# Optimization experiments

Measured on AMD Instinct MI355X. Metric: run time of the kernel, lower is better.

## Reference

```python
import jax, jax.numpy as jnp
import numpy as np


def l2norm(t, eps=1e-12):
    # matches F.normalize(p=2, dim=-1): divide by norm clamped to eps
    n = jnp.linalg.norm(t, axis=-1, keepdims=True)
    return t / jnp.maximum(n, eps)


def setup_inputs() -> dict:
    key = jax.random.key(0)
    kx, ke = jax.random.split(key)
    B, N, D, C = 8, 1024, 256, 8192
    x = jax.random.normal(kx, (B, N, D), dtype=jnp.float32)
    # codebook initialized l2-normalized, as in __init__ (kmeans_init=False)
    embed = l2norm(jax.random.normal(ke, (1, C, D), dtype=jnp.float32))
    return {"x": x, "embed": embed}


def reference(x, embed):
    # x: [B, N, D]; ndim < 4 -> add codebook dim h=1
    xh = x[None]                                   # [1, B, N, D]
    h, b, n, d = xh.shape
    flat = l2norm(xh.reshape(h, b * n, d))         # [1, B*N, D]
    e = l2norm(embed)                              # [1, C, D]
    # cosine-similarity distances
    dist = jnp.einsum('hnd,hcd->hnc', flat, e)     # [1, B*N, C]
    # sample_codebook_temp == 0 -> plain argmax
    idx = jnp.argmax(dist, axis=-1).reshape(h, b, n)  # [1, B, N]
    # batched_embedding: gather UN-normalized codebook rows
    quantize = jax.vmap(lambda em, ix: em[ix])(embed, idx)  # [1, B, N, D]
    # needs_codebook_dim -> strip leading dim
    return quantize[0], idx[0]
```

## Files before the change

### kernel.cpp

```cpp
#include <hip/hip_runtime.h>
#include <math.h>

#define QROWS 8192
#define DDIM  256
#define CCNT  8192

typedef __attribute__((ext_vector_type(4))) float f32x4;
typedef __attribute__((ext_vector_type(8))) short bf16x8;

__device__ __forceinline__ unsigned short f2bf(float f) {
    unsigned u = __float_as_uint(f);
    u += 0x7fffu + ((u >> 16) & 1u);
    return (unsigned short)(u >> 16);
}
__device__ __forceinline__ unsigned u32max(unsigned a, unsigned b) { return a > b ? a : b; }
__device__ __forceinline__ unsigned u32min(unsigned a, unsigned b) { return a < b ? a : b; }

__device__ __forceinline__ unsigned key32(float v, unsigned enc) {
    unsigned u = __float_as_uint(v);
    unsigned s = (unsigned)((int)u >> 31);
    return ((u ^ (s | 0x80000000u)) & 0xFFFFFF00u) | enc;
}

__global__ void k_prep(const float* __restrict__ x, unsigned short* __restrict__ xb,
                       const float* __restrict__ e, unsigned short* __restrict__ eb) {
    const int bid = blockIdx.x;
    if (bid < 1024) {
        const int i = (bid * 256 + threadIdx.x) * 8;
        const float4 f0 = *reinterpret_cast<const float4*>(x + i);
        const float4 f1 = *reinterpret_cast<const float4*>(x + i + 4);
        uint4 o;
        o.x = f2bf(f0.x) | ((unsigned)f2bf(f0.y) << 16);
        o.y = f2bf(f0.z) | ((unsigned)f2bf(f0.w) << 16);
        o.z = f2bf(f1.x) | ((unsigned)f2bf(f1.y) << 16);
        o.w = f2bf(f1.z) | ((unsigned)f2bf(f1.w) << 16);
        *reinterpret_cast<uint4*>(xb + i) = o;
    } else {
        const int row  = (bid - 1024) * 4 + (threadIdx.x >> 6);
        const int lane = threadIdx.x & 63;
        const float4 v = *reinterpret_cast<const float4*>(e + (size_t)row * DDIM + lane * 4);
        float s = v.x * v.x + v.y * v.y + v.z * v.z + v.w * v.w;
        #pragma unroll
        for (int off = 1; off < 64; off <<= 1) s += __shfl_xor(s, off);
        const float inv = 1.0f / fmaxf(sqrtf(s), 1e-12f);
        ushort4 o;
        o.x = f2bf(v.x * inv); o.y = f2bf(v.y * inv);
        o.z = f2bf(v.z * inv); o.w = f2bf(v.w * inv);
        *reinterpret_cast<ushort4*>(eb + (size_t)row * DDIM + lane * 4) = o;
    }
}

#define GLOAD_LDS(g, s) \
    __builtin_amdgcn_global_load_lds((const __attribute__((address_space(1))) void*)(g), \
                                     (__attribute__((address_space(3))) void*)(s), 16, 0, 0)

#define SBAR do { asm volatile("" ::: "memory"); __builtin_amdgcn_s_barrier(); \
                  asm volatile("" ::: "memory"); } while (0)
#define WAIT_LGKM(n) do { asm volatile("s_waitcnt lgkmcnt(" #n ")" ::: "memory"); \
                          __builtin_amdgcn_sched_barrier(0); } while (0)
#define WAIT_VM(n) do { asm volatile("s_waitcnt vmcnt(" #n ")" ::: "memory"); \
                        __builtin_amdgcn_sched_barrier(0); } while (0)

__launch_bounds__(512, 2)
__global__ void k_gemm(const unsigned short* __restrict__ xb,
                       const unsigned short* __restrict__ eb,
                       unsigned* pout ) {
    extern __shared__ char smem[];

    const int tid = threadIdx.x;
    const int w = tid >> 6, l = tid & 63;
    const int lg = l >> 4, lr = l & 15;
    const int bid = blockIdx.x;
    const int panel = (bid & 7) * 2 + ((bid >> 3) >> 4);
    const int split = (bid >> 3) & 15;
    const int n0 = panel * 512, c0 = split * 512;

    const int arl = w * 2 + (l >> 5);
    const size_t soff = (size_t)(((l & 31) ^ (arl & 7)) * 16);
    const char* gApro = (const char*)xb + (size_t)(n0 + arl) * 512 + soff;
    const char* gBpro = (const char*)eb + (size_t)(c0 + arl) * 512 + soff;
    const int wlds = w * 1024;

#define STAGEA(r) do { _Pragma("unroll") for (int g_ = 0; g_ < 4; ++g_)                    \
    GLOAD_LDS(gApro + (r) * 32768 + g_ * 8192,                                             \
              smem + ((r) & 1) * 32768 + g_ * 8192 + wlds); } while (0)
#define STAGEB(t) do { _Pragma("unroll") for (int g_ = 0; g_ < 2; ++g_)                    \
    GLOAD_LDS(gBpro + (size_t)(t) * 16384 + g_ * 8192,                                     \
              smem + 65536 + ((t) & 3) * 16384 + g_ * 8192 + wlds); } while (0)

    bf16x8 aF[4][8];
#define READA(slot) do { _Pragma("unroll") for (int mi_ = 0; mi_ < 4; ++mi_)               \
    _Pragma("unroll") for (int kk_ = 0; kk_ < 8; ++kk_)                                    \
        aF[mi_][kk_] = *reinterpret_cast<const bf16x8*>(smem + (slot) * 32768              \
            + (mi_ * 16 + lr) * 512 + (((kk_ * 4 + lg) ^ (lr & 7)) * 16)); } while (0)

    STAGEA(0); STAGEA(1);
    STAGEB(0); STAGEB(1); STAGEB(2); STAGEB(3);
    WAIT_VM(12); SBAR;  if (w == 0) READA(0);  WAIT_LGKM(0); SBAR; STAGEA(2);
    WAIT_VM(12); SBAR;  if (w == 1) READA(1);  WAIT_LGKM(0); SBAR; STAGEA(3);
    WAIT_VM(4);  SBAR;  if (w == 2) READA(0);  WAIT_LGKM(0); SBAR; STAGEA(4);
    WAIT_VM(4);  SBAR;  if (w == 3) READA(1);  WAIT_LGKM(0); SBAR; STAGEA(5);
    WAIT_VM(4);  SBAR;  if (w == 4) READA(0);  WAIT_LGKM(0); SBAR; STAGEA(6);
    WAIT_VM(4);  SBAR;  if (w == 5) READA(1);  WAIT_LGKM(0); SBAR; STAGEA(7);
    WAIT_VM(4);  SBAR;  if (w == 6) READA(0);  WAIT_LGKM(0); SBAR;
    WAIT_VM(0);  SBAR;  if (w == 7) READA(1);  WAIT_LGKM(0); SBAR;

    const f32x4 zf4 = {0.f, 0.f, 0.f, 0.f};
    f32x4 acc[4][2];
    #pragma unroll
    for (int i = 0; i < 4; ++i) { acc[i][0] = zf4; acc[i][1] = zf4; }
    unsigned rk1[16], rk2[16];
    #pragma unroll
    for (int i = 0; i < 16; ++i) { rk1[i] = 0u; rk2[i] = 0u; }
    bf16x8 bf[3][2];
    const int bcol0 = lr * 512;
    const int cxor = lr & 7;

#define FLUSH(half) do {                                                                   \
    _Pragma("unroll") for (int i_ = 0; i_ < 16; ++i_) {                                    \
        unsigned t1_ = rk1[i_], t2_ = rk2[i_];                                             \
        _Pragma("unroll") for (int off_ = 1; off_ < 16; off_ <<= 1) {                      \
            const unsigned o1_ = __shfl_xor(t1_, off_);                                    \
            const unsigned o2_ = __shfl_xor(t2_, off_);                                    \
            const unsigned n1_ = u32max(t1_, o1_), lo_ = u32min(t1_, o1_);                 \
            t2_ = u32max(u32max(t2_, o2_), lo_);                                           \
            t1_ = n1_;                                                                     \
        }                                                                                  \
        if (lr == 0) {                                                                     \
            const int row_ = n0 + w * 64 + (i_ >> 2) * 16 + lg * 4 + (i_ & 3);             \
            uint2 o_; o_.x = t1_; o_.y = t2_;                                              \
            *reinterpret_cast<uint2*>(pout + (size_t)row_ * 256 + split * 4 + (half) * 2) = o_; \
        }                                                                                  \
        rk1[i_] = 0u; rk2[i_] = 0u;                                                        \
    }                                                                                      \
} while (0)

    #pragma unroll 1
    for (int t = 0; t < 16; ++t) {
        if (t <= 13)      { WAIT_VM(4); }
        else if (t == 14) { WAIT_VM(2); }
        else              { WAIT_VM(0); }
        SBAR;
        if (t >= 1 && t < 13) STAGEB(t + 3);

        const char* sb = smem + 65536 + (t & 3) * 16384;
        #pragma unroll
        for (int nj = 0; nj < 2; ++nj)
            bf[0][nj] = *reinterpret_cast<const bf16x8*>(sb + nj * 8192 + bcol0 + ((lg ^ cxor) * 16));
        #pragma unroll
        for (int nj = 0; nj < 2; ++nj)
            bf[1][nj] = *reinterpret_cast<const bf16x8*>(sb + nj * 8192 + bcol0 + (((4 + lg) ^ cxor) * 16));

        #pragma unroll
        for (int kk = 0; kk < 8; ++kk) {
            if (kk < 6) {
                #pragma unroll
                for (int nj = 0; nj < 2; ++nj)
                    bf[(kk + 2) % 3][nj] = *reinterpret_cast<const bf16x8*>(
                        sb + nj * 8192 + bcol0 + ((((kk + 2) * 4 + lg) ^ cxor) * 16));
                WAIT_LGKM(4);
            } else if (kk == 6) { WAIT_LGKM(2); } else { WAIT_LGKM(0); }
            __builtin_amdgcn_s_setprio(1);
            #pragma unroll
            for (int mi = 0; mi < 4; ++mi)
                #pragma unroll
                for (int nj = 0; nj < 2; ++nj)
                    acc[mi][nj] = __builtin_amdgcn_mfma_f32_16x16x32_bf16(
                        aF[mi][kk], bf[kk % 3][nj], acc[mi][nj], 0, 0, 0);
            __builtin_amdgcn_s_setprio(0);
        }

        const unsigned encb = (unsigned)(255 - (t & 7) * 32) - (unsigned)lr;
        #pragma unroll
        for (int mi = 0; mi < 4; ++mi)
            #pragma unroll
            for (int rr = 0; rr < 4; ++rr) {
                const unsigned q0 = key32(acc[mi][0][rr], encb);
                const unsigned q1 = key32(acc[mi][1][rr], encb - 16u);
                const unsigned m01 = u32max(q0, q1), n01 = u32min(q0, q1);
                const int i = mi * 4 + rr;
                const unsigned lo = u32min(rk1[i], m01);
                rk1[i] = u32max(rk1[i], m01);
                rk2[i] = u32max(u32max(rk2[i], n01), lo);
                acc[mi][0][rr] = 0.0f; acc[mi][1][rr] = 0.0f;
            }
        if (t == 7) FLUSH(0);
        if (t == 15) FLUSH(1);
    }
#undef STAGEA
#undef STAGEB
#undef READA
#undef FLUSH
}

__global__ void k_fixup(const unsigned* pk,
                        const float* __restrict__ x, const float* __restrict__ e,
                        float* out) {
    const int row = blockIdx.x * 4 + (threadIdx.x >> 6);
    const int t   = threadIdx.x & 63;
    unsigned long long kk0 = 0ull, kk1 = 0ull;
    if (t < 32) {
        const uint2 kv = reinterpret_cast<const uint2*>(pk + (size_t)row * 256)[t];
        const int col0 = t * 256 + 255 - (int)(kv.x & 255u);
        kk0 = ((unsigned long long)(kv.x & 0xFFFFFF00u) << 32) | (unsigned)(~col0);
        const int col1 = t * 256 + 255 - (int)(kv.y & 255u);
        kk1 = ((unsigned long long)(kv.y & 0xFFFFFF00u) << 32) | (unsigned)(~col1);
    }

    int cand[4];
    #pragma unroll
    for (int p = 0; p < 4; ++p) {
        unsigned long long m = kk0 > kk1 ? kk0 : kk1;
        #pragma unroll
        for (int off = 1; off < 64; off <<= 1) {
            const unsigned long long o = __shfl_xor(m, off);
            if (o > m) m = o;
        }
        cand[p] = (int)(~(unsigned)m) & (CCNT - 1);
        if (kk0 == m) kk0 = 0ull;
        if (kk1 == m) kk1 = 0ull;
    }

    const float4 xv = *reinterpret_cast<const float4*>(x + (size_t)row * DDIM + t * 4);
    float best = -INFINITY; int bc = 0x7fffffff;
    #pragma unroll
    for (int p = 0; p < 4; ++p) {
        const int c = cand[p];
        const float4 ev = *reinterpret_cast<const float4*>(e + (size_t)c * DDIM + t * 4);
        float d  = xv.x * ev.x + xv.y * ev.y + xv.z * ev.z + xv.w * ev.w;
        float ss = ev.x * ev.x + ev.y * ev.y + ev.z * ev.z + ev.w * ev.w;
        #pragma unroll
        for (int off = 1; off < 64; off <<= 1) {
            d  += __shfl_xor(d, off);
            ss += __shfl_xor(ss, off);
        }
        const float v = d * (1.0f / fmaxf(sqrtf(ss), 1e-12f));
        if (v > best || (v == best && c < bc)) { best = v; bc = c; }
    }

    if (t == 0) out[(size_t)QROWS * DDIM + row] = (float)bc;
    const float4 q = *reinterpret_cast<const float4*>(e + (size_t)bc * DDIM + t * 4);
    *reinterpret_cast<float4*>(out + (size_t)row * DDIM + t * 4) = q;
}

extern "C" void kernel_launch(void* const* d_in, const int* in_sizes, int n_in,
                              void* d_out, int out_size, void* d_ws, size_t ws_size,
                              hipStream_t stream) {
    const float* x = (const float*)d_in[0];
    const float* e = (const float*)d_in[1];
    float* out = (float*)d_out;
    char* ws = (char*)d_ws;

    unsigned short* xb = (unsigned short*)ws;
    unsigned short* eb = (unsigned short*)(ws + (size_t)4 * 1024 * 1024);

    hipFuncSetAttribute(reinterpret_cast<const void*>(k_gemm),
                        hipFuncAttributeMaxDynamicSharedMemorySize, 131072);

    k_prep<<<3072, 256, 0, stream>>>(x, xb, e, eb);
    k_gemm<<<256, 512, 131072, stream>>>(xb, eb, (unsigned*)d_out);
    k_fixup<<<QROWS / 4, 256, 0, stream>>>((const unsigned*)d_out, x, e, out);
}
```

Baseline: 65.26 us.

## Restructure GEMM staging: two-phase A preload, 8-slot B ring, two tiles per barrier

Replaces the eight-step staggered A-fragment preload with two bulk half-loads that reuse the whole LDS, then turns all 128KB of LDS into an 8-slot ring for codebook (B) tiles. The main loop now handles two B tiles per barrier, with six tiles prefetched ahead, and drops the explicit register triple-buffering, lgkm waits and setprio around the MFMAs. The goal is fewer barriers and deeper global-load prefetch, at the cost of a serialized A-load prologue and leaving LDS-read scheduling to the compiler.

```diff
diff --git a/kernel.cpp b/kernel.cpp
--- a/kernel.cpp
+++ b/kernel.cpp
@@ -69,52 +69,72 @@
 
     const int tid = threadIdx.x;
     const int w = tid >> 6, l = tid & 63;
-    const int lg = l >> 4, lr = l & 15;
+    const int lg = l >> 4, lr = l & 15, lr7 = lr & 7;
     const int bid = blockIdx.x;
     const int panel = (bid & 7) * 2 + ((bid >> 3) >> 4);
     const int split = (bid >> 3) & 15;
     const int n0 = panel * 512, c0 = split * 512;
 
-    const int arl = w * 2 + (l >> 5);
-    const size_t soff = (size_t)(((l & 31) ^ (arl & 7)) * 16);
-    const char* gApro = (const char*)xb + (size_t)(n0 + arl) * 512 + soff;
-    const char* gBpro = (const char*)eb + (size_t)(c0 + arl) * 512 + soff;
-    const int wlds = w * 1024;
-
-#define STAGEA(r) do { _Pragma("unroll") for (int g_ = 0; g_ < 4; ++g_)                    \
-    GLOAD_LDS(gApro + (r) * 32768 + g_ * 8192,                                             \
-              smem + ((r) & 1) * 32768 + g_ * 8192 + wlds); } while (0)
+    const int lchk = (tid & 24) | ((tid & 7) ^ ((tid >> 5) & 7));
+    const char* baseA = (const char*)xb + (size_t)(n0 + (tid >> 5)) * 512 + lchk * 16;
+    const char* baseB = (const char*)eb + (size_t)(c0 + (tid >> 5)) * 512 + lchk * 16;
+    const int wl16 = w * 1024;
+
+#define STAGE_AHALF(h) do { _Pragma("unroll") for (int g_ = 0; g_ < 16; ++g_)              \
+    GLOAD_LDS(baseA + (h) * 131072 + g_ * 8192, smem + g_ * 8192 + wl16); } while (0)
 #define STAGEB(t) do { _Pragma("unroll") for (int g_ = 0; g_ < 2; ++g_)                    \
-    GLOAD_LDS(gBpro + (size_t)(t) * 16384 + g_ * 8192,                                     \
-              smem + 65536 + ((t) & 3) * 16384 + g_ * 8192 + wlds); } while (0)
+    GLOAD_LDS(baseB + (size_t)(t) * 16384 + g_ * 8192,                                     \
+              smem + ((t) & 7) * 16384 + g_ * 8192 + wl16); } while (0)
 
     bf16x8 aF[4][8];
-#define READA(slot) do { _Pragma("unroll") for (int mi_ = 0; mi_ < 4; ++mi_)               \
-    _Pragma("unroll") for (int kk_ = 0; kk_ < 8; ++kk_)                                    \
-        aF[mi_][kk_] = *reinterpret_cast<const bf16x8*>(smem + (slot) * 32768              \
-            + (mi_ * 16 + lr) * 512 + (((kk_ * 4 + lg) ^ (lr & 7)) * 16)); } while (0)
-
-    STAGEA(0); STAGEA(1);
-    STAGEB(0); STAGEB(1); STAGEB(2); STAGEB(3);
-    WAIT_VM(12); SBAR;  if (w == 0) READA(0);  WAIT_LGKM(0); SBAR; STAGEA(2);
-    WAIT_VM(12); SBAR;  if (w == 1) READA(1);  WAIT_LGKM(0); SBAR; STAGEA(3);
-    WAIT_VM(4);  SBAR;  if (w == 2) READA(0);  WAIT_LGKM(0); SBAR; STAGEA(4);
-    WAIT_VM(4);  SBAR;  if (w == 3) READA(1);  WAIT_LGKM(0); SBAR; STAGEA(5);
-    WAIT_VM(4);  SBAR;  if (w == 4) READA(0);  WAIT_LGKM(0); SBAR; STAGEA(6);
-    WAIT_VM(4);  SBAR;  if (w == 5) READA(1);  WAIT_LGKM(0); SBAR; STAGEA(7);
-    WAIT_VM(4);  SBAR;  if (w == 6) READA(0);  WAIT_LGKM(0); SBAR;
-    WAIT_VM(0);  SBAR;  if (w == 7) READA(1);  WAIT_LGKM(0); SBAR;
+#define READA() do { _Pragma("unroll") for (int mi_ = 0; mi_ < 4; ++mi_)                   \
+    _Pragma("unroll") for (int kk_ = 0; kk_ < 8; ++kk_) {                                  \
+        const int lc_ = kk_ * 4 + lg;                                                      \
+        const int ph_ = (lc_ & 24) | ((lc_ & 7) ^ lr7);                                    \
+        aF[mi_][kk_] = *reinterpret_cast<const bf16x8*>(                                   \
+            smem + ((w & 3) * 64 + mi_ * 16 + lr) * 512 + ph_ * 16); } } while (0)
+
+    STAGE_AHALF(0);
+    WAIT_VM(0); SBAR;
+    if (w < 4) READA();
+    WAIT_LGKM(0); SBAR;
+    STAGE_AHALF(1);
+    WAIT_VM(0); SBAR;
+    if (w >= 4) READA();
+    WAIT_LGKM(0); SBAR;
+    STAGEB(0); STAGEB(1); STAGEB(2); STAGEB(3); STAGEB(4); STAGEB(5);
 
     const f32x4 zf4 = {0.f, 0.f, 0.f, 0.f};
     f32x4 acc[4][2];
-    #pragma unroll
-    for (int i = 0; i < 4; ++i) { acc[i][0] = zf4; acc[i][1] = zf4; }
     unsigned rk1[16], rk2[16];
     #pragma unroll
     for (int i = 0; i < 16; ++i) { rk1[i] = 0u; rk2[i] = 0u; }
-    bf16x8 bf[3][2];
-    const int bcol0 = lr * 512;
-    const int cxor = lr & 7;
+
+#define TILE(t) do {                                                                       \
+    const char* sb_ = smem + ((t) & 7) * 16384;                                            \
+    _Pragma("unroll") for (int mi_ = 0; mi_ < 4; ++mi_)                                    \
+        { acc[mi_][0] = zf4; acc[mi_][1] = zf4; }                                          \
+    _Pragma("unroll") for (int kk_ = 0; kk_ < 8; ++kk_) {                                  \
+        const int lc_ = kk_ * 4 + lg;                                                      \
+        const int ph_ = ((lc_ & 24) | ((lc_ & 7) ^ lr7)) * 16;                             \
+        const bf16x8 b0_ = *reinterpret_cast<const bf16x8*>(sb_ + (lr) * 512 + ph_);       \
+        const bf16x8 b1_ = *reinterpret_cast<const bf16x8*>(sb_ + (16 + lr) * 512 + ph_);  \
+        _Pragma("unroll") for (int mi_ = 0; mi_ < 4; ++mi_) {                              \
+            acc[mi_][0] = __builtin_amdgcn_mfma_f32_16x16x32_bf16(aF[mi_][kk_], b0_, acc[mi_][0], 0, 0, 0); \
+            acc[mi_][1] = __builtin_amdgcn_mfma_f32_16x16x32_bf16(aF[mi_][kk_], b1_, acc[mi_][1], 0, 0, 0); \
+        } }                                                                                \
+    const unsigned encb_ = (unsigned)(255 - ((t) & 7) * 32) - (unsigned)lr;                \
+    _Pragma("unroll") for (int mi_ = 0; mi_ < 4; ++mi_)                                    \
+        _Pragma("unroll") for (int rr_ = 0; rr_ < 4; ++rr_) {                              \
+            const unsigned q0_ = key32(acc[mi_][0][rr_], encb_);                           \
+            const unsigned q1_ = key32(acc[mi_][1][rr_], encb_ - 16u);                     \
+            const unsigned m01_ = u32max(q0_, q1_), n01_ = u32min(q0_, q1_);               \
+            const int i_ = mi_ * 4 + rr_;                                                  \
+            const unsigned lo_ = u32min(rk1[i_], m01_);                                    \
+            rk1[i_] = u32max(rk1[i_], m01_);                                               \
+            rk2[i_] = u32max(u32max(rk2[i_], n01_), lo_);                                  \
+        }                                                                                  \
+} while (0)
 
 #define FLUSH(half) do {                                                                   \
     _Pragma("unroll") for (int i_ = 0; i_ < 16; ++i_) {                                    \
@@ -136,60 +156,21 @@
 } while (0)
 
     #pragma unroll 1
-    for (int t = 0; t < 16; ++t) {
-        if (t <= 13)      { WAIT_VM(4); }
-        else if (t == 14) { WAIT_VM(2); }
-        else              { WAIT_VM(0); }
+    for (int u = 0; u < 8; ++u) {
+        if (u < 6)       { WAIT_VM(8); }
+        else if (u == 6) { WAIT_VM(4); }
+        else             { WAIT_VM(0); }
         SBAR;
-        if (t >= 1 && t < 13) STAGEB(t + 3);
-
-        const char* sb = smem + 65536 + (t & 3) * 16384;
-        #pragma unroll
-        for (int nj = 0; nj < 2; ++nj)
-            bf[0][nj] = *reinterpret_cast<const bf16x8*>(sb + nj * 8192 + bcol0 + ((lg ^ cxor) * 16));
-        #pragma unroll
-        for (int nj = 0; nj < 2; ++nj)
-            bf[1][nj] = *reinterpret_cast<const bf16x8*>(sb + nj * 8192 + bcol0 + (((4 + lg) ^ cxor) * 16));
-
-        #pragma unroll
-        for (int kk = 0; kk < 8; ++kk) {
-            if (kk < 6) {
-                #pragma unroll
-                for (int nj = 0; nj < 2; ++nj)
-                    bf[(kk + 2) % 3][nj] = *reinterpret_cast<const bf16x8*>(
-                        sb + nj * 8192 + bcol0 + ((((kk + 2) * 4 + lg) ^ cxor) * 16));
-                WAIT_LGKM(4);
-            } else if (kk == 6) { WAIT_LGKM(2); } else { WAIT_LGKM(0); }
-            __builtin_amdgcn_s_setprio(1);
-            #pragma unroll
-            for (int mi = 0; mi < 4; ++mi)
-                #pragma unroll
-                for (int nj = 0; nj < 2; ++nj)
-                    acc[mi][nj] = __builtin_amdgcn_mfma_f32_16x16x32_bf16(
-                        aF[mi][kk], bf[kk % 3][nj], acc[mi][nj], 0, 0, 0);
-            __builtin_amdgcn_s_setprio(0);
-        }
-
-        const unsigned encb = (unsigned)(255 - (t & 7) * 32) - (unsigned)lr;
-        #pragma unroll
-        for (int mi = 0; mi < 4; ++mi)
-            #pragma unroll
-            for (int rr = 0; rr < 4; ++rr) {
-                const unsigned q0 = key32(acc[mi][0][rr], encb);
-                const unsigned q1 = key32(acc[mi][1][rr], encb - 16u);
-                const unsigned m01 = u32max(q0, q1), n01 = u32min(q0, q1);
-                const int i = mi * 4 + rr;
-                const unsigned lo = u32min(rk1[i], m01);
-                rk1[i] = u32max(rk1[i], m01);
-                rk2[i] = u32max(u32max(rk2[i], n01), lo);
-                acc[mi][0][rr] = 0.0f; acc[mi][1][rr] = 0.0f;
-            }
-        if (t == 7) FLUSH(0);
-        if (t == 15) FLUSH(1);
-    }
-#undef STAGEA
+        if (u < 5) { STAGEB(2 * u + 6); STAGEB(2 * u + 7); }
+        TILE(2 * u);
+        TILE(2 * u + 1);
+        if (u == 3) FLUSH(0);
+        if (u == 7) FLUSH(1);
+    }
+#undef STAGE_AHALF
 #undef STAGEB
 #undef READA
+#undef TILE
 #undef FLUSH
 }
 
```

Result: faster. 60.27 us (-7.6%).
